# Optimization experiments

Measured on AMD Instinct MI355X. Metric: run time of the kernel, lower is better.

## Reference

```python
import jax, jax.numpy as jnp
import numpy as np

_SAMPLING_EPS = 1e-5


def setup_inputs() -> dict:
    key = jax.random.key(0)
    k1, k2, k3, k4, k5 = jax.random.split(key, 5)
    B, V = 128, 128000
    logits = jax.random.normal(k1, (B, V), dtype=jnp.float32)
    temperature = jax.random.uniform(k2, (B,), dtype=jnp.float32)  # some rows < eps -> greedy
    top_k = jax.random.randint(k3, (B,), 1, 64, dtype=jnp.int32)   # in [1, 63]
    top_p = jax.random.uniform(k4, (B,), dtype=jnp.float32, minval=0.05, maxval=1.0)
    noise_u = jax.random.uniform(k5, (B, V), dtype=jnp.float32, minval=1e-10, maxval=1.0)
    return {"logits": logits, "temperature": temperature, "top_k": top_k,
            "top_p": top_p, "noise_u": noise_u, "max_num_logprobs": 5}


def _apply_top_k_top_p(logits, k, p):
    # Faithful to vLLM: ascending sort, top-k threshold mask, top-p cumsum mask, scatter back.
    B, V = logits.shape
    order = jnp.argsort(logits, axis=-1)                       # ascending, [B, V]
    logits_sort = jnp.take_along_axis(logits, order, axis=-1)
    neg_inf = jnp.float32(-jnp.inf)
    # top-k: pivot value at position V - k; everything strictly below it -> -inf
    pivot_idx = (V - k.astype(jnp.int32))[:, None]             # [B, 1]
    pivot = jnp.take_along_axis(logits_sort, pivot_idx, axis=-1)
    logits_sort = jnp.where(logits_sort < pivot, neg_inf, logits_sort)
    # top-p: softmax over sorted logits, cumsum, drop prefix with mass <= 1 - p (keep last)
    probs_sort = jax.nn.softmax(logits_sort, axis=-1)
    probs_sum = jnp.cumsum(probs_sort, axis=-1)
    top_p_mask = probs_sum <= (1.0 - p)[:, None]
    top_p_mask = top_p_mask.at[:, -1].set(False)
    logits_sort = jnp.where(top_p_mask, neg_inf, logits_sort)
    # scatter back to original vocab order
    rows = jnp.arange(B)[:, None]
    return jnp.zeros_like(logits).at[rows, order].set(logits_sort)


def reference(logits, temperature, top_k, top_p, noise_u, max_num_logprobs):
    # temperature scaling (temp < eps means greedy; divide by 1.0 instead)
    temp = jnp.where(temperature < _SAMPLING_EPS, 1.0, temperature)
    logits = logits.astype(jnp.float32) / temp[:, None]
    # top-k / top-p filtering
    logits = _apply_top_k_top_p(logits, top_k, top_p)
    # probabilities and sampling
    probs = jax.nn.softmax(logits, axis=-1)
    greedy = jnp.argmax(probs, axis=-1)
    q = -jnp.log(noise_u)                                      # Exp(1) noise (q.exponential_())
    random = jnp.argmax(probs / q, axis=-1)
    sampled = jnp.where(temperature < _SAMPLING_EPS, greedy, random).astype(jnp.int32)
    # top-k logprobs
    logprobs = jax.nn.log_softmax(logits, axis=-1)
    topk_logprobs, topk_indices = jax.lax.top_k(logprobs, max_num_logprobs)
    return sampled, topk_indices.astype(jnp.int32), topk_logprobs
```

## Files before the change

### kernel.cpp

```cpp
#include <hip/hip_runtime.h>
#include <math.h>
#include <stdint.h>

#define BT    256
#define TOPC  64
#define FT    512
#define SLOTS 32
#define CAP2  4096

__device__ __forceinline__ unsigned f2ord(float f) {
    unsigned u = __float_as_uint(f);
    return u ^ ((u & 0x80000000u) ? 0xFFFFFFFFu : 0x80000000u);
}
__device__ __forceinline__ float ord2f(unsigned k) {
    unsigned u = (k & 0x80000000u) ? (k ^ 0x80000000u) : (k ^ 0xFFFFFFFFu);
    return __uint_as_float(u);
}

__device__ unsigned radix_select_compact4(uint2* s_buf, uint2* s_keep,
                                          unsigned (*s_hist)[16], unsigned* p_cnt2,
                                          unsigned n, int tid, int wid)
{
    unsigned prefix = 0u;
    int remaining = TOPC;
    for (int shift = 28; shift >= 0; shift -= 4) {
        if (tid < 64) ((unsigned*)s_hist)[tid] = 0u;
        __syncthreads();
        for (unsigned i = (unsigned)tid; i < n; i += BT) {
            unsigned k = s_buf[i].x;
            bool ing = (shift == 28) || ((k >> (shift + 4)) == (prefix >> (shift + 4)));
            if (ing) atomicAdd(&s_hist[wid][(k >> shift) & 15u], 1u);
        }
        __syncthreads();
        int cum = 0; int b = 0; unsigned hb = 0u;
        for (int bb = 15; bb >= 0; --bb) {
            unsigned h = s_hist[0][bb] + s_hist[1][bb] + s_hist[2][bb] + s_hist[3][bb];
            cum += (int)h;
            if (cum >= remaining) { b = bb; hb = h; break; }
        }
        remaining -= (cum - (int)hb);
        prefix |= ((unsigned)b) << shift;
        __syncthreads();
    }
    if (tid == 0) *p_cnt2 = 0u;
    __syncthreads();
    for (unsigned i = (unsigned)tid; i < n; i += BT) {
        uint2 c = s_buf[i];
        if (c.x > prefix) s_keep[atomicAdd(p_cnt2, 1u)] = c;
    }
    __syncthreads();
    for (unsigned i = (unsigned)tid; i < n; i += BT) {
        uint2 c = s_buf[i];
        if (c.x == prefix) {
            unsigned pos = atomicAdd(p_cnt2, 1u);
            if (pos < TOPC) s_keep[pos] = c;
        }
    }
    __syncthreads();
    return prefix;
}

__global__ __launch_bounds__(64) void row_thresh(
    const float* __restrict__ logits, unsigned* __restrict__ thr,
    unsigned* __restrict__ ovf, int V)
{
    const int r    = blockIdx.x;
    const int lane = threadIdx.x;
    const float* rowp = logits + (size_t)r * (size_t)V;

    unsigned kr[64];
    #pragma unroll
    for (int g = 0; g < 8; ++g) {
        int c0 = g * 512 + lane * 8;
        if (c0 < V) {
            float4 a = *(const float4*)(rowp + c0);
            float4 b = *(const float4*)(rowp + c0 + 4);
            kr[g * 8 + 0] = f2ord(a.x); kr[g * 8 + 1] = f2ord(a.y);
            kr[g * 8 + 2] = f2ord(a.z); kr[g * 8 + 3] = f2ord(a.w);
            kr[g * 8 + 4] = f2ord(b.x); kr[g * 8 + 5] = f2ord(b.y);
            kr[g * 8 + 6] = f2ord(b.z); kr[g * 8 + 7] = f2ord(b.w);
        } else {
            #pragma unroll
            for (int j = 0; j < 8; ++j) kr[g * 8 + j] = 0u;
        }
    }

    unsigned lo = 0u, hi = 0xFFFFu;
    while (lo < hi) {
        unsigned mid = (lo + hi + 1u) >> 1;
        unsigned t = mid << 16;
        int c = 0;
        #pragma unroll
        for (int j = 0; j < 64; ++j) c += __popcll(__ballot(kr[j] >= t));
        if (c >= TOPC) lo = mid; else hi = mid - 1u;
    }
    if (lane == 0) { thr[r] = lo << 16; ovf[r] = 0u; }
}

__global__ __launch_bounds__(BT) void filter_pass(
    const float* __restrict__ logits, const unsigned* __restrict__ thr,
    unsigned* __restrict__ ovf, uint2* __restrict__ surv,
    int B, int V, int tpr, int slots)
{
    const int tid  = threadIdx.x;
    const int wid  = tid >> 6;
    const int lane = tid & 63;
    const unsigned long long ltm = (1ull << lane) - 1ull;
    const int nw = gridDim.x * (BT / 64);
    const int ntiles = B * tpr;

    for (int tw = blockIdx.x * (BT / 64) + wid; tw < ntiles; tw += nw) {
        const int t    = __builtin_amdgcn_readfirstlane(tw);
        const int row  = t / tpr;
        const int tin  = t - row * tpr;
        const int col0 = tin * FT + lane * 8;
        const bool v   = col0 < V;
        const float* rowp = logits + (size_t)row * (size_t)V;

        unsigned k[8];
        if (v) {
            float4 a = *(const float4*)(rowp + col0);
            float4 b = *(const float4*)(rowp + col0 + 4);
            k[0] = f2ord(a.x); k[1] = f2ord(a.y); k[2] = f2ord(a.z); k[3] = f2ord(a.w);
            k[4] = f2ord(b.x); k[5] = f2ord(b.y); k[6] = f2ord(b.z); k[7] = f2ord(b.w);
        } else {
            #pragma unroll
            for (int j = 0; j < 8; ++j) k[j] = 0u;
        }

        const unsigned tr = thr[row];
        uint2* base = surv + (size_t)t * (unsigned)slots;

        unsigned tot = 0u;
        #pragma unroll
        for (int j = 0; j < 8; ++j) {
            bool pa = v && (k[j] >= tr);
            unsigned long long m = __ballot(pa);
            if (pa) {
                unsigned pos = tot + (unsigned)__popcll(m & ltm);
                if (pos < (unsigned)slots)
                    base[pos] = make_uint2(k[j], (unsigned)(col0 + j));
            }
            tot += (unsigned)__popcll(m);
        }
        if (lane < slots && (unsigned)lane >= tot)
            base[lane] = make_uint2(0u, 0u);
        if (lane == 0 && tot > (unsigned)slots)
            atomicOr(&ovf[row], 1u);
    }
}

__global__ __launch_bounds__(BT) void phase2_sample(
    const uint2* __restrict__ surv, const unsigned* __restrict__ ovf,
    const unsigned* __restrict__ thr, const float* __restrict__ logits,
    const float* __restrict__ temperature,
    const int*   __restrict__ top_k,
    const float* __restrict__ top_p,
    const float* __restrict__ noise_u,
    float* __restrict__ out,
    int B, int V, int M, int tpr, int slots)
{
    __shared__ uint2    s_buf[CAP2];
    __shared__ uint2    s_keep[TOPC];
    __shared__ unsigned s_hist[4][16];
    __shared__ unsigned s_cnt, s_cnt2, s_ovf;
    __shared__ float    sval[TOPC], se[TOPC], sq[TOPC];
    __shared__ int      sidx[TOPC];

    const int r    = blockIdx.x;
    const int tid  = threadIdx.x;
    const int wid  = tid >> 6;
    const int lane = tid & 63;
    const unsigned long long ltm = (1ull << lane) - 1ull;

    const unsigned tr = thr[r];
    bool fb = (ovf[r] != 0u);
    unsigned n = 0u;

    if (!fb) {
        if (tid == 0) s_cnt = 0u;
        __syncthreads();
        const uint2* rs = surv + (size_t)r * (unsigned)(tpr * slots);
        const int tslots = tpr * slots;
        for (int i = tid; i < tslots; i += BT) {
            uint2 c = rs[i];
            bool pass = (c.x >= tr);
            unsigned long long m = __ballot(pass);
            if (m) {
                int leader = __ffsll((unsigned long long)m) - 1;
                unsigned b0 = 0u;
                if (lane == leader)
                    b0 = atomicAdd(&s_cnt, (unsigned)__popcll(m));
                b0 = __shfl(b0, leader);
                if (pass) {
                    unsigned pos = b0 + (unsigned)__popcll(m & ltm);
                    if (pos < CAP2) s_buf[pos] = c;
                }
            }
        }
        __syncthreads();
        n = s_cnt;
        if (n > CAP2) fb = true;
        __syncthreads();
    }

    if (fb) {
        const float* rowp = logits + (size_t)r * (size_t)V;
        if (tid == 0) { s_cnt = 0u; s_ovf = 0u; }
        __syncthreads();
        unsigned vst = tr;
        bool strict = false;
        for (int t = 0; t < V; t += BT * 8) {
            int bs = t + tid * 8;
            bool v = bs < V;
            unsigned kk[8];
            if (v) {
                float4 a = *(const float4*)(rowp + bs);
                float4 b = *(const float4*)(rowp + bs + 4);
                kk[0] = f2ord(a.x); kk[1] = f2ord(a.y); kk[2] = f2ord(a.z); kk[3] = f2ord(a.w);
                kk[4] = f2ord(b.x); kk[5] = f2ord(b.y); kk[6] = f2ord(b.z); kk[7] = f2ord(b.w);
            } else {
                #pragma unroll
                for (int j = 0; j < 8; ++j) kk[j] = 0u;
            }
            unsigned pm = 0u; int np = 0;
            if (v) {
                #pragma unroll
                for (int j = 0; j < 8; ++j) {
                    bool pa = strict ? (kk[j] > vst) : (kk[j] >= vst);
                    if (pa) { pm |= (1u << j); ++np; }
                }
            }
            for (;;) {
                if (np) {
                    unsigned pos = atomicAdd(&s_cnt, (unsigned)np);
                    unsigned rem = 0u; int nr = 0;
                    #pragma unroll
                    for (int j = 0; j < 8; ++j) {
                        if (pm & (1u << j)) {
                            if (pos < CAP2) s_buf[pos] = make_uint2(kk[j], (unsigned)(bs + j));
                            else { rem |= (1u << j); ++nr; }
                            ++pos;
                        }
                    }
                    if (nr) s_ovf = 1u;
                    pm = rem; np = nr;
                }
                __syncthreads();
                unsigned o = s_ovf;
                __syncthreads();
                if (!o) break;
                unsigned nn = s_cnt; if (nn > CAP2) nn = CAP2;
                unsigned v2s = radix_select_compact4(s_buf, s_keep, s_hist, &s_cnt2,
                                                     nn, tid, wid);
                if (tid < TOPC) s_buf[tid] = s_keep[tid];
                if (tid == 0) { s_cnt = TOPC; s_ovf = 0u; }
                __syncthreads();
                unsigned rem = 0u; int nr = 0;
                #pragma unroll
                for (int j = 0; j < 8; ++j)
                    if ((pm & (1u << j)) && kk[j] > v2s) { rem |= (1u << j); ++nr; }
                pm = rem; np = nr;
                vst = v2s; strict = true;
            }
        }
        n = s_cnt; if (n > CAP2) n = CAP2;
    }

    if (n < TOPC) {
        for (unsigned i = n + (unsigned)tid; i < TOPC; i += BT)
            s_buf[i] = make_uint2(0u, 0u);
        n = TOPC;
        __syncthreads();
    }

    radix_select_compact4(s_buf, s_keep, s_hist, &s_cnt2, n, tid, wid);

    for (int kk = 2; kk <= TOPC; kk <<= 1) {
        for (int j = kk >> 1; j > 0; j >>= 1) {
            if (tid < TOPC / 2) {
                int i0 = ((tid & ~(j - 1)) << 1) | (tid & (j - 1));
                int i1 = i0 | j;
                bool up = ((i0 & kk) == 0);
                uint2 A = s_keep[i0], Bv = s_keep[i1];
                bool gt = (A.x < Bv.x) || (A.x == Bv.x && A.y > Bv.y);
                if (gt == up) { s_keep[i0] = Bv; s_keep[i1] = A; }
            }
            __syncthreads();
        }
    }

    float temp_orig = temperature[r];
    float temp = (temp_orig < 1e-5f) ? 1.0f : temp_orig;

    if (tid < TOPC) {
        unsigned k = s_keep[tid].x;
        int id = (int)s_keep[tid].y;
        sval[tid] = ord2f(k) / temp;
        sidx[tid] = id;
        float u = noise_u[(size_t)r * (size_t)V + id];
        sq[tid] = -logf(u);
    }
    __syncthreads();
    if (tid < TOPC) se[tid] = expf(sval[tid] - sval[0]);
    __syncthreads();

    if (tid == 0) {
        int k = top_k[r];
        if (k < 1) k = 1; if (k > TOPC) k = TOPC;
        float p = top_p[r];

        float pivot = sval[k - 1];
        int m = k;
        while (m < TOPC && sval[m] >= pivot) ++m;

        float sum = 0.f;
        for (int i = 0; i < m; ++i) sum += se[i];

        float thr1 = 1.0f - p;
        float S = 0.f;
        int f = 1;
        for (int i = m - 1; i >= 1; --i) {
            S += se[i] / sum;
            if (S > thr1) { f = i + 1; break; }
        }

        float sum2 = 0.f;
        for (int i = 0; i < f; ++i) sum2 += se[i];

        int greedy = sidx[0];
        float best = -1.f; int bidx = 0x7fffffff;
        for (int i = 0; i < f; ++i) {
            float ratio = (se[i] / sum2) / sq[i];
            if (ratio > best || (ratio == best && sidx[i] < bidx)) {
                best = ratio; bidx = sidx[i];
            }
        }
        int sampled = (temp_orig < 1e-5f) ? greedy : bidx;

        float lse = logf(sum2);
        out[r] = (float)sampled;
        float* oidx = out + B + (size_t)r * M;
        float* olp  = out + B + (size_t)B * M + (size_t)r * M;
        int produced = 0;
        for (int i = 0; i < f && produced < M; ++i, ++produced) {
            oidx[produced] = (float)sidx[i];
            olp[produced]  = (sval[i] - sval[0]) - lse;
        }
        int v = 0;
        while (produced < M) {
            bool used = false;
            for (int i = 0; i < f; ++i) if (sidx[i] == v) { used = true; break; }
            if (!used) { oidx[produced] = (float)v; olp[produced] = -3.0e38f; ++produced; }
            ++v;
        }
    }
}

extern "C" void kernel_launch(void* const* d_in, const int* in_sizes, int n_in,
                              void* d_out, int out_size, void* d_ws, size_t ws_size,
                              hipStream_t stream)
{
    const float* logits      = (const float*)d_in[0];
    const float* temperature = (const float*)d_in[1];
    const int*   top_k       = (const int*)d_in[2];
    const float* top_p       = (const float*)d_in[3];
    const float* noise_u     = (const float*)d_in[4];

    const int B = in_sizes[1];
    const int V = in_sizes[0] / B;
    const int M = (out_size / B - 1) / 2;

    const int tpr = (V + FT - 1) / FT;

    unsigned* thr = (unsigned*)d_ws;
    unsigned* ovf = thr + B;
    size_t off = (((size_t)2 * B * sizeof(unsigned)) + 7) & ~(size_t)7;
    uint2* surv = (uint2*)((char*)d_ws + off);

    int slots = SLOTS;
    if (ws_size > off) {
        size_t avail = (ws_size - off) / ((size_t)B * tpr * sizeof(uint2));
        if (avail < (size_t)slots) slots = (int)avail;
    } else slots = 1;
    if (slots < 1) slots = 1;

    const int ntiles = B * tpr;
    int fblocks = (ntiles + 3) / 4;
    if (fblocks > 2048) fblocks = 2048;

    row_thresh<<<B, 64, 0, stream>>>(logits, thr, ovf, V);
    filter_pass<<<fblocks, BT, 0, stream>>>(logits, thr, ovf, surv,
                                            B, V, tpr, slots);
    phase2_sample<<<B, BT, 0, stream>>>(surv, ovf, thr, logits,
                                        temperature, top_k, top_p, noise_u,
                                        (float*)d_out, B, V, M, tpr, slots);
}
```

Before: 199.6 us.

## Split per-row candidate reduction into parallel partition kernel before final sampling

```diff
diff --git a/kernel.cpp b/kernel.cpp
--- a/kernel.cpp
+++ b/kernel.cpp
@@ -2,11 +2,13 @@
 #include <math.h>
 #include <stdint.h>
 
-#define BT    256
-#define TOPC  64
-#define FT    512
-#define SLOTS 32
-#define CAP2  4096
+#define BT     256
+#define TOPC   64
+#define FT     512
+#define SLOTS  32
+#define NPART  8
+#define CAPR   4096
+#define CAPF   1024
 
 __device__ __forceinline__ unsigned f2ord(float f) {
     unsigned u = __float_as_uint(f);
@@ -150,65 +152,76 @@
     }
 }
 
-__global__ __launch_bounds__(BT) void phase2_sample(
-    const uint2* __restrict__ surv, const unsigned* __restrict__ ovf,
+__global__ __launch_bounds__(BT) void reduce_slots(
+    const uint2* __restrict__ surv, uint2* __restrict__ cand,
+    int tpr, int slots, int npart)
+{
+    __shared__ uint2    s_buf[CAPR];
+    __shared__ uint2    s_keep[TOPC];
+    __shared__ unsigned s_hist[4][16];
+    __shared__ unsigned s_cnt2;
+
+    const int r    = blockIdx.y;
+    const int part = blockIdx.x;
+    const int tid  = threadIdx.x;
+    const int wid  = tid >> 6;
+
+    const int tslots = tpr * slots;
+    const int share  = (tslots + npart - 1) / npart;
+    const int start  = part * share;
+    int end = start + share; if (end > tslots) end = tslots;
+    int nn = end - start; if (nn < 0) nn = 0;
+
+    const uint2* rs = surv + (size_t)r * (unsigned)tslots + start;
+    for (int i = tid; i < nn; i += BT)
+        s_buf[i] = rs[i];
+    unsigned n = (unsigned)nn;
+    if (n < TOPC) {
+        for (unsigned i = n + (unsigned)tid; i < TOPC; i += BT)
+            s_buf[i] = make_uint2(0u, 0u);
+        n = TOPC;
+    }
+    __syncthreads();
+
+    radix_select_compact4(s_buf, s_keep, s_hist, &s_cnt2, n, tid, wid);
+    if (tid < TOPC)
+        cand[((size_t)r * (unsigned)npart + (unsigned)part) * TOPC + tid] = s_keep[tid];
+}
+
+__global__ __launch_bounds__(BT) void phase2_final(
+    const uint2* __restrict__ cand, const unsigned* __restrict__ ovf,
     const unsigned* __restrict__ thr, const float* __restrict__ logits,
     const float* __restrict__ temperature,
     const int*   __restrict__ top_k,
     const float* __restrict__ top_p,
     const float* __restrict__ noise_u,
     float* __restrict__ out,
-    int B, int V, int M, int tpr, int slots)
-{
-    __shared__ uint2    s_buf[CAP2];
+    int B, int V, int M, int nc)
+{
+    __shared__ uint2    s_buf[CAPF];
     __shared__ uint2    s_keep[TOPC];
     __shared__ unsigned s_hist[4][16];
     __shared__ unsigned s_cnt, s_cnt2, s_ovf;
     __shared__ float    sval[TOPC], se[TOPC], sq[TOPC];
     __shared__ int      sidx[TOPC];
 
-    const int r    = blockIdx.x;
-    const int tid  = threadIdx.x;
-    const int wid  = tid >> 6;
-    const int lane = tid & 63;
-    const unsigned long long ltm = (1ull << lane) - 1ull;
-
-    const unsigned tr = thr[r];
-    bool fb = (ovf[r] != 0u);
-    unsigned n = 0u;
+    const int r   = blockIdx.x;
+    const int tid = threadIdx.x;
+    const int wid = tid >> 6;
+
+    const bool fb = (ovf[r] != 0u);
+    unsigned n;
 
     if (!fb) {
-        if (tid == 0) s_cnt = 0u;
+        n = (unsigned)nc;
+        for (unsigned i = (unsigned)tid; i < n; i += BT)
+            s_buf[i] = cand[(size_t)r * (unsigned)nc + i];
         __syncthreads();
-        const uint2* rs = surv + (size_t)r * (unsigned)(tpr * slots);
-        const int tslots = tpr * slots;
-        for (int i = tid; i < tslots; i += BT) {
-            uint2 c = rs[i];
-            bool pass = (c.x >= tr);
-            unsigned long long m = __ballot(pass);
-            if (m) {
-                int leader = __ffsll((unsigned long long)m) - 1;
-                unsigned b0 = 0u;
-                if (lane == leader)
-                    b0 = atomicAdd(&s_cnt, (unsigned)__popcll(m));
-                b0 = __shfl(b0, leader);
-                if (pass) {
-                    unsigned pos = b0 + (unsigned)__popcll(m & ltm);
-                    if (pos < CAP2) s_buf[pos] = c;
-                }
-            }
-        }
-        __syncthreads();
-        n = s_cnt;
-        if (n > CAP2) fb = true;
-        __syncthreads();
-    }
-
-    if (fb) {
+    } else {
         const float* rowp = logits + (size_t)r * (size_t)V;
         if (tid == 0) { s_cnt = 0u; s_ovf = 0u; }
         __syncthreads();
-        unsigned vst = tr;
+        unsigned vst = thr[r];
         bool strict = false;
         for (int t = 0; t < V; t += BT * 8) {
             int bs = t + tid * 8;
@@ -238,7 +251,7 @@
                     #pragma unroll
                     for (int j = 0; j < 8; ++j) {
                         if (pm & (1u << j)) {
-                            if (pos < CAP2) s_buf[pos] = make_uint2(kk[j], (unsigned)(bs + j));
+                            if (pos < CAPF) s_buf[pos] = make_uint2(kk[j], (unsigned)(bs + j));
                             else { rem |= (1u << j); ++nr; }
                             ++pos;
                         }
@@ -250,9 +263,9 @@
                 unsigned o = s_ovf;
                 __syncthreads();
                 if (!o) break;
-                unsigned nn = s_cnt; if (nn > CAP2) nn = CAP2;
+                unsigned nn2 = s_cnt; if (nn2 > CAPF) nn2 = CAPF;
                 unsigned v2s = radix_select_compact4(s_buf, s_keep, s_hist, &s_cnt2,
-                                                     nn, tid, wid);
+                                                     nn2, tid, wid);
                 if (tid < TOPC) s_buf[tid] = s_keep[tid];
                 if (tid == 0) { s_cnt = TOPC; s_ovf = 0u; }
                 __syncthreads();
@@ -264,14 +277,13 @@
                 vst = v2s; strict = true;
             }
         }
-        n = s_cnt; if (n > CAP2) n = CAP2;
-    }
-
-    if (n < TOPC) {
-        for (unsigned i = n + (unsigned)tid; i < TOPC; i += BT)
-            s_buf[i] = make_uint2(0u, 0u);
-        n = TOPC;
-        __syncthreads();
+        n = s_cnt; if (n > CAPF) n = CAPF;
+        if (n < TOPC) {
+            for (unsigned i = n + (unsigned)tid; i < TOPC; i += BT)
+                s_buf[i] = make_uint2(0u, 0u);
+            n = TOPC;
+            __syncthreads();
+        }
     }
 
     radix_select_compact4(s_buf, s_keep, s_hist, &s_cnt2, n, tid, wid);
@@ -375,12 +387,14 @@
 
     unsigned* thr = (unsigned*)d_ws;
     unsigned* ovf = thr + B;
-    size_t off = (((size_t)2 * B * sizeof(unsigned)) + 7) & ~(size_t)7;
-    uint2* surv = (uint2*)((char*)d_ws + off);
+    size_t off1 = (((size_t)2 * B * sizeof(unsigned)) + 7) & ~(size_t)7;
+    uint2* cand = (uint2*)((char*)d_ws + off1);
+    size_t off2 = off1 + (size_t)B * NPART * TOPC * sizeof(uint2);
+    uint2* surv = (uint2*)((char*)d_ws + off2);
 
     int slots = SLOTS;
-    if (ws_size > off) {
-        size_t avail = (ws_size - off) / ((size_t)B * tpr * sizeof(uint2));
+    if (ws_size > off2) {
+        size_t avail = (ws_size - off2) / ((size_t)B * tpr * sizeof(uint2));
         if (avail < (size_t)slots) slots = (int)avail;
     } else slots = 1;
     if (slots < 1) slots = 1;
@@ -392,7 +406,9 @@
     row_thresh<<<B, 64, 0, stream>>>(logits, thr, ovf, V);
     filter_pass<<<fblocks, BT, 0, stream>>>(logits, thr, ovf, surv,
                                             B, V, tpr, slots);
-    phase2_sample<<<B, BT, 0, stream>>>(surv, ovf, thr, logits,
-                                        temperature, top_k, top_p, noise_u,
-                                        (float*)d_out, B, V, M, tpr, slots);
-}
+    dim3 gr(NPART, B);
+    reduce_slots<<<gr, BT, 0, stream>>>(surv, cand, tpr, slots, NPART);
+    phase2_final<<<B, BT, 0, stream>>>(cand, ovf, thr, logits,
+                                       temperature, top_k, top_p, noise_u,
+                                       (float*)d_out, B, V, M, NPART * TOPC);
+}
```

New measurement: 193.5 us. -3.1%, faster.
